# Kernel tuning notes

Hardware: AMD Instinct MI355X
Metric: run time of the kernel (lower is better)

The kernel has to match this reference:

```python
import jax, jax.numpy as jnp
import numpy as np

GROUP_SIZE = 128
NIBBLES = 8  # int4 values packed per int32


def dequantize(qweight, qzeros, scales):
    """Unpack int4 weights/zeros and dequantize: w = (q - z) * scale.

    qweight: [in/8, out] int32, 8 int4 values packed along the IN dim.
    qzeros:  [groups, out/8] int32, 8 int4 zeros packed along the OUT dim.
    scales:  [groups, out] fp16.
    Returns w: [in, out] fp16.
    """
    shifts = (jnp.arange(NIBBLES, dtype=jnp.int32) * 4)
    # unpack weights along input dim -> [in/8, 8, out] -> [in, out]
    q = ((qweight[:, None, :] >> shifts[None, :, None]) & 15)
    q = q.reshape(-1, qweight.shape[1])
    # unpack zeros along output dim -> [groups, out/8, 8] -> [groups, out]
    z = ((qzeros[:, :, None] >> shifts[None, None, :]) & 15)
    z = z.reshape(qzeros.shape[0], -1)
    # broadcast per-group zeros/scales to per-input-row
    z_full = jnp.repeat(z, GROUP_SIZE, axis=0).astype(scales.dtype)   # [in, out]
    s_full = jnp.repeat(scales, GROUP_SIZE, axis=0)                    # [in, out]
    return (q.astype(scales.dtype) - z_full) * s_full


def setup_inputs() -> dict:
    key = jax.random.key(0)
    k1, k2, k3, k4, k5 = jax.random.split(key, 5)
    B, S, IN, OUT, G = 2, 2048, 4096, 11008, 32
    x = jax.random.normal(k1, (B, S, IN), dtype=jnp.float16)
    qweight = jax.random.randint(k2, (IN // 8, OUT), 0, 2147483647, dtype=jnp.int32)
    qzeros = jax.random.randint(k3, (G, OUT // 8), 0, 2147483647, dtype=jnp.int32)
    scales = jax.random.uniform(k4, (G, OUT), dtype=jnp.float16, minval=0.001, maxval=0.02)
    bias = jax.random.normal(k5, (OUT,), dtype=jnp.float16)
    return {"x": x, "qweight": qweight, "qzeros": qzeros, "scales": scales, "bias": bias}


def reference(x, qweight, qzeros, scales, bias):
    w = dequantize(qweight, qzeros, scales)  # [in, out] fp16
    # q4_matmul accumulates in fp32, emits fp16
    out = jnp.einsum('bsi,io->bso', x, w, preferred_element_type=jnp.float32)
    out = out.astype(jnp.float16) + bias
    return out
```

## Files before the change

kernel.cpp:

```cpp
#include <hip/hip_runtime.h>
#include <cstdint>
#include <cstddef>


typedef unsigned short u16;
typedef u16    u16x8  __attribute__((ext_vector_type(8)));
typedef __bf16 bfv8   __attribute__((ext_vector_type(8)));
typedef float  f32x4  __attribute__((ext_vector_type(4)));

#define K_DIM 4096
#define N_DIM 11008
#define GS    128
#define KT    (K_DIM / 64)
#define LSTR  72

__device__ __forceinline__ u16 f2bf(float f) {
  union { float f; uint32_t u; } v;
  v.f = f;
  uint32_t u = v.u + 0x7FFFu + ((v.u >> 16) & 1u);
  return (u16)(u >> 16);
}
__device__ __forceinline__ float f16r(float v) {
  return (float)(_Float16)v;
}
__device__ __forceinline__ void async_load16(const u16* g, u16* l) {
  __builtin_amdgcn_global_load_lds(
      (const __attribute__((address_space(1))) uint32_t*)g,
      (__attribute__((address_space(3))) uint32_t*)l, 16, 0, 0);
}

__global__ __launch_bounds__(256) void convert_x_tiled(
    const float* __restrict__ x, u16* __restrict__ xb) {
  const int kt = blockIdx.x, mt = blockIdx.y;
  const int k0 = kt * 64, m0 = mt * 128;
  u16* dst = xb + ((size_t)(mt * KT + kt)) * 8192;
#pragma unroll
  for (int i = 0; i < 4; ++i) {
    const int g  = i * 256 + threadIdx.x;
    const int nl = g >> 3;
    const int cg = (g & 7) ^ (nl & 7);
    const float* sp = x + (size_t)(m0 + nl) * K_DIM + (k0 + cg * 8);
    const f32x4 p = *(const f32x4*)sp;
    const f32x4 q = *(const f32x4*)(sp + 4);
    u16x8 o;
#pragma unroll
    for (int t = 0; t < 4; ++t) { o[t] = f2bf(p[t]); o[t + 4] = f2bf(q[t]); }
    *(u16x8*)(dst + (size_t)g * 8) = o;
  }
}

__global__ __launch_bounds__(256) void dequant_tiled(
    const uint32_t* __restrict__ qweight, const uint32_t* __restrict__ qzeros,
    const float* __restrict__ scales, u16* __restrict__ wt) {
  const int kt = blockIdx.x, nt = blockIdx.y;
  const int k0 = kt * 64, n0 = nt * 128;
  const int gq = kt >> 1;
  u16* dst = wt + ((size_t)(nt * KT + kt)) * 8192;
#pragma unroll
  for (int i = 0; i < 4; ++i) {
    const int g  = i * 256 + threadIdx.x;
    const int nl = g >> 3;
    const int cg = (g & 7) ^ (nl & 7);
    const int n  = n0 + nl;
    const uint32_t zq = qzeros[(size_t)gq * (N_DIM / 8) + (n >> 3)];
    const int   z   = (int)((zq >> ((n & 7) * 4)) & 15u);
    const float s   = scales[(size_t)gq * N_DIM + n];
    const float nzs = -s * (float)z;
    const uint32_t q = qweight[(size_t)(k0 / 8 + cg) * N_DIM + n];
    u16x8 o;
#pragma unroll
    for (int t = 0; t < 8; ++t) {
      const int qv = (int)((q >> (t * 4)) & 15u);
      o[t] = f2bf(fmaf((float)qv, s, nzs));
    }
    *(u16x8*)(dst + (size_t)g * 8) = o;
  }
}

__global__ __launch_bounds__(256) void gemm_tiled(
    const u16* __restrict__ xb, const u16* __restrict__ wt,
    const float* __restrict__ bias, float* __restrict__ out) {
  __shared__ __align__(16) u16 As[8192];
  __shared__ __align__(16) u16 Bs[8192];

  const int tid  = threadIdx.x;
  const int lane = tid & 63;
  const int wave = tid >> 6;
  const int n0 = blockIdx.x * 128;
  const int m0 = blockIdx.y * 128;

  const int m_off = (wave >> 1) * 64;
  const int n_off = (wave & 1) * 64;
  const int lrow  = lane & 15;
  const int lk    = lane >> 4;
  const int sw    = lrow & 7;

  const u16* abase = xb + (size_t)blockIdx.y * KT * 8192;
  const u16* bbase = wt + (size_t)blockIdx.x * KT * 8192;

  f32x4 acc[4][4];
#pragma unroll
  for (int i = 0; i < 4; ++i)
#pragma unroll
    for (int j = 0; j < 4; ++j) acc[i][j] = f32x4{0.f, 0.f, 0.f, 0.f};

  for (int kt = 0; kt < KT; ++kt) {
    const u16* ag = abase + (size_t)kt * 8192;
    const u16* bg = bbase + (size_t)kt * 8192;
#pragma unroll
    for (int i = 0; i < 4; ++i) {
      async_load16(ag + (size_t)(i * 256 + tid) * 8,
                   As + (size_t)(i * 256 + wave * 64) * 8);
      async_load16(bg + (size_t)(i * 256 + tid) * 8,
                   Bs + (size_t)(i * 256 + wave * 64) * 8);
    }
    __syncthreads();

#pragma unroll
    for (int ks = 0; ks < 2; ++ks) {
      const int kq = ks * 4 + lk;
      const int c = (kq ^ sw) * 8;
      bfv8 a[4], b[4];
#pragma unroll
      for (int i = 0; i < 4; ++i) {
        const int mf = m_off + i * 16 + lrow;
        a[i] = __builtin_bit_cast(bfv8, *(const u16x8*)&As[mf * 64 + c]);
      }
#pragma unroll
      for (int j = 0; j < 4; ++j) {
        const int nf = n_off + j * 16 + lrow;
        b[j] = __builtin_bit_cast(bfv8, *(const u16x8*)&Bs[nf * 64 + c]);
      }
#pragma unroll
      for (int i = 0; i < 4; ++i)
#pragma unroll
        for (int j = 0; j < 4; ++j)
          acc[i][j] = __builtin_amdgcn_mfma_f32_16x16x32_bf16(a[i], b[j],
                                                              acc[i][j], 0, 0, 0);
    }
    __syncthreads();
  }

#pragma unroll
  for (int j = 0; j < 4; ++j) {
    const int n = n0 + n_off + j * 16 + lrow;
    const float bvf = bias[n];
#pragma unroll
    for (int i = 0; i < 4; ++i) {
      const int mrow = m0 + m_off + i * 16 + lk * 4;
#pragma unroll
      for (int r = 0; r < 4; ++r) {
        out[(size_t)(mrow + r) * N_DIM + n] = f16r(f16r(acc[i][j][r]) + bvf);
      }
    }
  }
}

__global__ __launch_bounds__(256) void gemm_fused(
    const float* __restrict__ xf, const uint32_t* __restrict__ qw,
    const uint32_t* __restrict__ qzeros, const float* __restrict__ scales,
    const float* __restrict__ bias, float* __restrict__ out) {
  __shared__ __align__(16) u16 As[128 * LSTR];
  __shared__ __align__(16) u16 Bs[128 * LSTR];

  const int tid  = threadIdx.x;
  const int lane = tid & 63;
  const int wave = tid >> 6;
  const int n0 = blockIdx.x * 128;
  const int m0 = blockIdx.y * 128;
  const int m_off = (wave >> 1) * 64;
  const int n_off = (wave & 1) * 64;
  const int lrow  = lane & 15;
  const int lk    = lane >> 4;
  const int sm = tid >> 3;
  const int sc = tid & 7;

  f32x4 acc[4][4];
#pragma unroll
  for (int i = 0; i < 4; ++i)
#pragma unroll
    for (int j = 0; j < 4; ++j) acc[i][j] = f32x4{0.f, 0.f, 0.f, 0.f};

  const int ncol = n0 + (tid & 127);
  float s_cur = 0.f, nzs_cur = 0.f;

  for (int kt = 0; kt < KT; ++kt) {
    const int k0 = kt * 64;
    u16x8 av[4];
#pragma unroll
    for (int i = 0; i < 4; ++i) {
      const int m = i * 32 + sm;
      const float* sp = xf + (size_t)(m0 + m) * K_DIM + (k0 + sc * 8);
      const f32x4 p = *(const f32x4*)sp;
      const f32x4 q4 = *(const f32x4*)(sp + 4);
#pragma unroll
      for (int t = 0; t < 4; ++t) { av[i][t] = f2bf(p[t]); av[i][t+4] = f2bf(q4[t]); }
    }
    u16x8 bv[4];
    if ((k0 & (GS - 1)) == 0) {
      const int g = k0 >> 7;
      const uint32_t zq = qzeros[(size_t)g * (N_DIM / 8) + (ncol >> 3)];
      const int z = (int)((zq >> ((ncol & 7) * 4)) & 15u);
      s_cur = scales[(size_t)g * N_DIM + ncol];
      nzs_cur = -s_cur * (float)z;
    }
#pragma unroll
    for (int i = 0; i < 4; ++i) {
      const int k8l = (tid >> 7) + i * 2;
      const uint32_t q = qw[(size_t)(k0 / 8 + k8l) * N_DIM + ncol];
#pragma unroll
      for (int t = 0; t < 8; ++t) {
        const int qv = (int)((q >> (t * 4)) & 15u);
        bv[i][t] = f2bf(fmaf((float)qv, s_cur, nzs_cur));
      }
    }
#pragma unroll
    for (int i = 0; i < 4; ++i)
      *(u16x8*)&As[(i * 32 + sm) * LSTR + sc * 8] = av[i];
    {
      const int nl = tid & 127;
#pragma unroll
      for (int i = 0; i < 4; ++i) {
        const int k8l = (tid >> 7) + i * 2;
        *(u16x8*)&Bs[nl * LSTR + k8l * 8] = bv[i];
      }
    }
    __syncthreads();
#pragma unroll
    for (int ks = 0; ks < 2; ++ks) {
      const int c = (ks * 4 + lk) * 8;
      bfv8 a[4], b[4];
#pragma unroll
      for (int i = 0; i < 4; ++i)
        a[i] = __builtin_bit_cast(bfv8,
                 *(const u16x8*)&As[(m_off + i * 16 + lrow) * LSTR + c]);
#pragma unroll
      for (int j = 0; j < 4; ++j)
        b[j] = __builtin_bit_cast(bfv8,
                 *(const u16x8*)&Bs[(n_off + j * 16 + lrow) * LSTR + c]);
#pragma unroll
      for (int i = 0; i < 4; ++i)
#pragma unroll
        for (int j = 0; j < 4; ++j)
          acc[i][j] = __builtin_amdgcn_mfma_f32_16x16x32_bf16(a[i], b[j],
                                                              acc[i][j], 0, 0, 0);
    }
    __syncthreads();
  }
#pragma unroll
  for (int j = 0; j < 4; ++j) {
    const int n = n0 + n_off + j * 16 + lrow;
    const float bvf = bias[n];
#pragma unroll
    for (int i = 0; i < 4; ++i) {
      const int mrow = m0 + m_off + i * 16 + lk * 4;
#pragma unroll
      for (int r = 0; r < 4; ++r)
        out[(size_t)(mrow + r) * N_DIM + n] = f16r(f16r(acc[i][j][r]) + bvf);
    }
  }
}

extern "C" void kernel_launch(void* const* d_in, const int* in_sizes, int n_in,
                              void* d_out, int out_size, void* d_ws, size_t ws_size,
                              hipStream_t stream) {
  const float* x = nullptr;      const uint32_t* qweight = nullptr;
  const uint32_t* qzeros = nullptr;
  const float* scales = nullptr; const float* bias = nullptr;
  int M = 4096;
  for (int i = 0; i < n_in; ++i) {
    const long long s = in_sizes[i];
    if      (s == (long long)(K_DIM / 8) * N_DIM) qweight = (const uint32_t*)d_in[i];
    else if (s == (long long)(K_DIM / GS) * (N_DIM / 8)) qzeros = (const uint32_t*)d_in[i];
    else if (s == (long long)(K_DIM / GS) * N_DIM) scales = (const float*)d_in[i];
    else if (s == (long long)N_DIM) bias = (const float*)d_in[i];
    else { x = (const float*)d_in[i]; M = (int)(s / K_DIM); }
  }
  float* out = (float*)d_out;

  const size_t xb_bytes = (size_t)M * K_DIM * sizeof(u16);
  const size_t wt_bytes = (size_t)N_DIM * K_DIM * sizeof(u16);

  if (ws_size >= xb_bytes + wt_bytes) {
    u16* xbp = (u16*)d_ws;
    u16* wtp = (u16*)((char*)d_ws + xb_bytes);
    convert_x_tiled<<<dim3(KT, M / 128), 256, 0, stream>>>(x, xbp);
    dequant_tiled<<<dim3(KT, N_DIM / 128), 256, 0, stream>>>(
        qweight, qzeros, scales, wtp);
    gemm_tiled<<<dim3(N_DIM / 128, M / 128), 256, 0, stream>>>(
        xbp, wtp, bias, out);
  } else {
    gemm_fused<<<dim3(N_DIM / 128, M / 128), 256, 0, stream>>>(
        x, qweight, qzeros, scales, bias, out);
  }
}
```

Baseline: 741.8 us.

## Use 256x256 GEMM tiles with a four-stage async LDS pipeline

Measured after the change: 620.8 us. 16.3% less time.

```diff
diff --git a/kernel.cpp b/kernel.cpp
--- a/kernel.cpp
+++ b/kernel.cpp
@@ -11,7 +11,7 @@
 #define K_DIM 4096
 #define N_DIM 11008
 #define GS    128
-#define KT    (K_DIM / 64)
+#define KT32  (K_DIM / 32)
 #define LSTR  72
 
 __device__ __forceinline__ u16 f2bf(float f) {
@@ -29,17 +29,17 @@
       (__attribute__((address_space(3))) uint32_t*)l, 16, 0, 0);
 }
 
-__global__ __launch_bounds__(256) void convert_x_tiled(
+__global__ __launch_bounds__(256) void convert_x32(
     const float* __restrict__ x, u16* __restrict__ xb) {
   const int kt = blockIdx.x, mt = blockIdx.y;
-  const int k0 = kt * 64, m0 = mt * 128;
-  u16* dst = xb + ((size_t)(mt * KT + kt)) * 8192;
-#pragma unroll
-  for (int i = 0; i < 4; ++i) {
-    const int g  = i * 256 + threadIdx.x;
-    const int nl = g >> 3;
-    const int cg = (g & 7) ^ (nl & 7);
-    const float* sp = x + (size_t)(m0 + nl) * K_DIM + (k0 + cg * 8);
+  const int m0 = mt * 128, k0 = kt * 32;
+  u16* dst = xb + ((size_t)mt * KT32 + kt) * 4096;
+#pragma unroll
+  for (int i = 0; i < 2; ++i) {
+    const int g = i * 256 + threadIdx.x;
+    const int r = g >> 2, s = g & 3;
+    const int kq = s ^ ((r >> 1) & 3);
+    const float* sp = x + (size_t)(m0 + r) * K_DIM + (k0 + kq * 8);
     const f32x4 p = *(const f32x4*)sp;
     const f32x4 q = *(const f32x4*)(sp + 4);
     u16x8 o;
@@ -49,105 +49,132 @@
   }
 }
 
-__global__ __launch_bounds__(256) void dequant_tiled(
+__global__ __launch_bounds__(256) void dequant32(
     const uint32_t* __restrict__ qweight, const uint32_t* __restrict__ qzeros,
     const float* __restrict__ scales, u16* __restrict__ wt) {
   const int kt = blockIdx.x, nt = blockIdx.y;
-  const int k0 = kt * 64, n0 = nt * 128;
-  const int gq = kt >> 1;
-  u16* dst = wt + ((size_t)(nt * KT + kt)) * 8192;
-#pragma unroll
-  for (int i = 0; i < 4; ++i) {
-    const int g  = i * 256 + threadIdx.x;
-    const int nl = g >> 3;
-    const int cg = (g & 7) ^ (nl & 7);
-    const int n  = n0 + nl;
+  const int n0 = nt * 128;
+  const int gq = kt >> 2;
+  u16* dst = wt + ((size_t)nt * KT32 + kt) * 4096;
+#pragma unroll
+  for (int i = 0; i < 2; ++i) {
+    const int g = i * 256 + threadIdx.x;
+    const int r = g >> 2, s = g & 3;
+    const int kq = s ^ ((r >> 1) & 3);
+    const int n = n0 + r;
     const uint32_t zq = qzeros[(size_t)gq * (N_DIM / 8) + (n >> 3)];
     const int   z   = (int)((zq >> ((n & 7) * 4)) & 15u);
-    const float s   = scales[(size_t)gq * N_DIM + n];
-    const float nzs = -s * (float)z;
-    const uint32_t q = qweight[(size_t)(k0 / 8 + cg) * N_DIM + n];
+    const float sc  = scales[(size_t)gq * N_DIM + n];
+    const float nzs = -sc * (float)z;
+    const uint32_t q = qweight[(size_t)(kt * 4 + kq) * N_DIM + n];
     u16x8 o;
 #pragma unroll
     for (int t = 0; t < 8; ++t) {
       const int qv = (int)((q >> (t * 4)) & 15u);
-      o[t] = f2bf(fmaf((float)qv, s, nzs));
+      o[t] = f2bf(fmaf((float)qv, sc, nzs));
     }
     *(u16x8*)(dst + (size_t)g * 8) = o;
   }
 }
 
-__global__ __launch_bounds__(256) void gemm_tiled(
+#define STAGE_A(t) do {                                                      \
+    const int sb_ = (t) & 3;                                                 \
+    async_load16(atile + ((size_t)0 * KT32 + (t)) * 4096 + tid * 8,          \
+                 As + sb_ * 8192 + 0 * 4096 + wave * 512);                   \
+    async_load16(atile + ((size_t)1 * KT32 + (t)) * 4096 + tid * 8,          \
+                 As + sb_ * 8192 + 1 * 4096 + wave * 512);                   \
+  } while (0)
+#define STAGE_B(t) do {                                                      \
+    const int sb_ = (t) & 3;                                                 \
+    async_load16(btile + ((size_t)0 * KT32 + (t)) * 4096 + tid * 8,          \
+                 Bs + sb_ * 8192 + 0 * 4096 + wave * 512);                   \
+    async_load16(btile + ((size_t)1 * KT32 + (t)) * 4096 + tid * 8,          \
+                 Bs + sb_ * 8192 + 1 * 4096 + wave * 512);                   \
+  } while (0)
+#define LDF(base, off) __builtin_bit_cast(bfv8, *(const u16x8*)((base) + (off)))
+#define MF(i, j, av, bv)                                                     \
+  acc[i][j] = __builtin_amdgcn_mfma_f32_16x16x32_bf16((av), (bv), acc[i][j], 0, 0, 0)
+
+__global__ __launch_bounds__(512, 2) void gemm_256(
     const u16* __restrict__ xb, const u16* __restrict__ wt,
     const float* __restrict__ bias, float* __restrict__ out) {
-  __shared__ __align__(16) u16 As[8192];
-  __shared__ __align__(16) u16 Bs[8192];
+  __shared__ __align__(16) u16 As[4 * 8192];
+  __shared__ __align__(16) u16 Bs[4 * 8192];
 
   const int tid  = threadIdx.x;
   const int lane = tid & 63;
   const int wave = tid >> 6;
-  const int n0 = blockIdx.x * 128;
-  const int m0 = blockIdx.y * 128;
-
-  const int m_off = (wave >> 1) * 64;
-  const int n_off = (wave & 1) * 64;
-  const int lrow  = lane & 15;
-  const int lk    = lane >> 4;
-  const int sw    = lrow & 7;
-
-  const u16* abase = xb + (size_t)blockIdx.y * KT * 8192;
-  const u16* bbase = wt + (size_t)blockIdx.x * KT * 8192;
-
-  f32x4 acc[4][4];
-#pragma unroll
-  for (int i = 0; i < 4; ++i)
+  const int wm   = wave >> 2;
+  const int wn   = wave & 3;
+  const int lrow = lane & 15;
+  const int lk   = lane >> 4;
+  const int swz  = (lrow >> 1) & 3;
+
+  const int n0 = blockIdx.x * 256;
+  const int m0 = blockIdx.y * 256;
+
+  const u16* atile = xb + (size_t)(2 * blockIdx.y) * KT32 * 4096;
+  const u16* btile = wt + (size_t)(2 * blockIdx.x) * KT32 * 4096;
+
+  const int aoff = wm * 4096 + (lrow * 4 + (lk ^ swz)) * 8;
+  const int boff = (wn >> 1) * 4096 + (((wn & 1) * 64 + lrow) * 4 + (lk ^ swz)) * 8;
+
+  f32x4 acc[8][4];
+#pragma unroll
+  for (int i = 0; i < 8; ++i)
 #pragma unroll
     for (int j = 0; j < 4; ++j) acc[i][j] = f32x4{0.f, 0.f, 0.f, 0.f};
 
-  for (int kt = 0; kt < KT; ++kt) {
-    const u16* ag = abase + (size_t)kt * 8192;
-    const u16* bg = bbase + (size_t)kt * 8192;
-#pragma unroll
-    for (int i = 0; i < 4; ++i) {
-      async_load16(ag + (size_t)(i * 256 + tid) * 8,
-                   As + (size_t)(i * 256 + wave * 64) * 8);
-      async_load16(bg + (size_t)(i * 256 + tid) * 8,
-                   Bs + (size_t)(i * 256 + wave * 64) * 8);
-    }
-    __syncthreads();
-
-#pragma unroll
-    for (int ks = 0; ks < 2; ++ks) {
-      const int kq = ks * 4 + lk;
-      const int c = (kq ^ sw) * 8;
-      bfv8 a[4], b[4];
-#pragma unroll
-      for (int i = 0; i < 4; ++i) {
-        const int mf = m_off + i * 16 + lrow;
-        a[i] = __builtin_bit_cast(bfv8, *(const u16x8*)&As[mf * 64 + c]);
-      }
-#pragma unroll
-      for (int j = 0; j < 4; ++j) {
-        const int nf = n_off + j * 16 + lrow;
-        b[j] = __builtin_bit_cast(bfv8, *(const u16x8*)&Bs[nf * 64 + c]);
-      }
-#pragma unroll
-      for (int i = 0; i < 4; ++i)
-#pragma unroll
-        for (int j = 0; j < 4; ++j)
-          acc[i][j] = __builtin_amdgcn_mfma_f32_16x16x32_bf16(a[i], b[j],
-                                                              acc[i][j], 0, 0, 0);
-    }
-    __syncthreads();
+  STAGE_A(0); STAGE_B(0); STAGE_A(1); STAGE_B(1); STAGE_A(2); STAGE_B(2);
+  asm volatile("s_waitcnt vmcnt(8)" ::: "memory");
+  asm volatile("s_barrier" ::: "memory");
+
+#pragma unroll 4
+  for (int t = 0; t < KT32; ++t) {
+    const u16* A = As + (t & 3) * 8192;
+    const u16* B = Bs + (t & 3) * 8192;
+    bfv8 a[4], b[4];
+#pragma unroll
+    for (int j = 0; j < 4; ++j) b[j] = LDF(B, boff + j * 512);
+#pragma unroll
+    for (int i = 0; i < 4; ++i) a[i] = LDF(A, aoff + i * 512);
+    if (t + 3 < KT32) STAGE_A(t + 3);
+    asm volatile("s_barrier" ::: "memory");
+    __builtin_amdgcn_s_setprio(1);
+#pragma unroll
+    for (int i = 0; i < 4; ++i)
+#pragma unroll
+      for (int j = 0; j < 4; ++j) MF(i, j, a[i], b[j]);
+    __builtin_amdgcn_s_setprio(0);
+    asm volatile("s_barrier" ::: "memory");
+#pragma unroll
+    for (int i = 0; i < 4; ++i) a[i] = LDF(A, aoff + (4 + i) * 512);
+    if (t + 3 < KT32) STAGE_B(t + 3);
+    asm volatile("s_barrier" ::: "memory");
+    __builtin_amdgcn_s_setprio(1);
+#pragma unroll
+    for (int i = 0; i < 4; ++i)
+#pragma unroll
+      for (int j = 0; j < 4; ++j) MF(4 + i, j, a[i], b[j]);
+    __builtin_amdgcn_s_setprio(0);
+    if (t == KT32 - 1) break;
+    if (t < KT32 - 3) {
+      asm volatile("s_waitcnt vmcnt(8)" ::: "memory");
+    } else if (t == KT32 - 3) {
+      asm volatile("s_waitcnt vmcnt(4)" ::: "memory");
+    } else {
+      asm volatile("s_waitcnt vmcnt(0)" ::: "memory");
+    }
+    asm volatile("s_barrier" ::: "memory");
   }
 
 #pragma unroll
   for (int j = 0; j < 4; ++j) {
-    const int n = n0 + n_off + j * 16 + lrow;
+    const int n = n0 + wn * 64 + j * 16 + lrow;
     const float bvf = bias[n];
 #pragma unroll
-    for (int i = 0; i < 4; ++i) {
-      const int mrow = m0 + m_off + i * 16 + lk * 4;
+    for (int i = 0; i < 8; ++i) {
+      const int mrow = m0 + wm * 128 + i * 16 + lk * 4;
 #pragma unroll
       for (int r = 0; r < 4; ++r) {
         out[(size_t)(mrow + r) * N_DIM + n] = f16r(f16r(acc[i][j][r]) + bvf);
@@ -184,7 +211,7 @@
   const int ncol = n0 + (tid & 127);
   float s_cur = 0.f, nzs_cur = 0.f;
 
-  for (int kt = 0; kt < KT; ++kt) {
+  for (int kt = 0; kt < K_DIM / 64; ++kt) {
     const int k0 = kt * 64;
     u16x8 av[4];
 #pragma unroll
@@ -281,16 +308,16 @@
   const size_t xb_bytes = (size_t)M * K_DIM * sizeof(u16);
   const size_t wt_bytes = (size_t)N_DIM * K_DIM * sizeof(u16);
 
-  if (ws_size >= xb_bytes + wt_bytes) {
+  if (ws_size >= xb_bytes + wt_bytes && (M % 256) == 0) {
     u16* xbp = (u16*)d_ws;
     u16* wtp = (u16*)((char*)d_ws + xb_bytes);
-    convert_x_tiled<<<dim3(KT, M / 128), 256, 0, stream>>>(x, xbp);
-    dequant_tiled<<<dim3(KT, N_DIM / 128), 256, 0, stream>>>(
+    convert_x32<<<dim3(KT32, M / 128), 256, 0, stream>>>(x, xbp);
+    dequant32<<<dim3(KT32, N_DIM / 128), 256, 0, stream>>>(
         qweight, qzeros, scales, wtp);
-    gemm_tiled<<<dim3(N_DIM / 128, M / 128), 256, 0, stream>>>(
+    gemm_256<<<dim3(N_DIM / 256, M / 256), 512, 0, stream>>>(
         xbp, wtp, bias, out);
   } else {
-    gemm_fused<<<dim3(N_DIM / 128, M / 128), 256, 0, stream>>>(
+    gemm_fused<<<dim3(N_DIM / 128, (M + 127) / 128), 256, 0, stream>>>(
         x, qweight, qzeros, scales, bias, out);
   }
 }
```

## Replace 128x128 GEMM with double-buffered 256x256 pipelined MFMA kernel

Applied to the files above, without the earlier changes.

Measured after the change: 614.3 us. 1.21x faster.

```diff
diff --git a/kernel.cpp b/kernel.cpp
--- a/kernel.cpp
+++ b/kernel.cpp
@@ -11,7 +11,7 @@
 #define K_DIM 4096
 #define N_DIM 11008
 #define GS    128
-#define KT    (K_DIM / 64)
+#define KT64  (K_DIM / 64)
 #define LSTR  72
 
 __device__ __forceinline__ u16 f2bf(float f) {
@@ -33,7 +33,7 @@
     const float* __restrict__ x, u16* __restrict__ xb) {
   const int kt = blockIdx.x, mt = blockIdx.y;
   const int k0 = kt * 64, m0 = mt * 128;
-  u16* dst = xb + ((size_t)(mt * KT + kt)) * 8192;
+  u16* dst = xb + ((size_t)(mt * KT64 + kt)) * 8192;
 #pragma unroll
   for (int i = 0; i < 4; ++i) {
     const int g  = i * 256 + threadIdx.x;
@@ -53,9 +53,9 @@
     const uint32_t* __restrict__ qweight, const uint32_t* __restrict__ qzeros,
     const float* __restrict__ scales, u16* __restrict__ wt) {
   const int kt = blockIdx.x, nt = blockIdx.y;
-  const int k0 = kt * 64, n0 = nt * 128;
+  const int n0 = nt * 128;
   const int gq = kt >> 1;
-  u16* dst = wt + ((size_t)(nt * KT + kt)) * 8192;
+  u16* dst = wt + ((size_t)(nt * KT64 + kt)) * 8192;
 #pragma unroll
   for (int i = 0; i < 4; ++i) {
     const int g  = i * 256 + threadIdx.x;
@@ -66,7 +66,7 @@
     const int   z   = (int)((zq >> ((n & 7) * 4)) & 15u);
     const float s   = scales[(size_t)gq * N_DIM + n];
     const float nzs = -s * (float)z;
-    const uint32_t q = qweight[(size_t)(k0 / 8 + cg) * N_DIM + n];
+    const uint32_t q = qweight[(size_t)(kt * 8 + cg) * N_DIM + n];
     u16x8 o;
 #pragma unroll
     for (int t = 0; t < 8; ++t) {
@@ -77,77 +77,125 @@
   }
 }
 
-__global__ __launch_bounds__(256) void gemm_tiled(
+#define LDF(p) __builtin_bit_cast(bfv8, *(const u16x8*)(p))
+#define BAR()  asm volatile("s_barrier" ::: "memory")
+#define VMW(n) asm volatile("s_waitcnt vmcnt(" #n ")" ::: "memory")
+
+#define STAGE_AH(ktt, h) do {                                                 \
+    const u16* s_ = at0 + ((size_t)(h) * KT64 + (ktt)) * 8192;                \
+    u16* d_ = &As[(((ktt) & 1) * 16384) + (h) * 8192 + wave * 512];           \
+    async_load16(s_ + (size_t)tid * 8, d_);                                   \
+    async_load16(s_ + (size_t)(512 + tid) * 8, d_ + 4096);                    \
+  } while (0)
+#define STAGE_BH(ktt, h) do {                                                 \
+    const u16* s_ = bt0 + ((size_t)(h) * KT64 + (ktt)) * 8192;                \
+    u16* d_ = &Bs[(((ktt) & 1) * 16384) + (h) * 8192 + wave * 512];           \
+    async_load16(s_ + (size_t)tid * 8, d_);                                   \
+    async_load16(s_ + (size_t)(512 + tid) * 8, d_ + 4096);                    \
+  } while (0)
+
+#define RD_AP(v, ib, sbx) do {                                                \
+    v[0] = LDF(&As[(sbx) * 16384 + aoff + (ib) * 1024 + kq0]);                \
+    v[1] = LDF(&As[(sbx) * 16384 + aoff + (ib) * 1024 + kq1]);                \
+    v[2] = LDF(&As[(sbx) * 16384 + aoff + ((ib) + 1) * 1024 + kq0]);          \
+    v[3] = LDF(&As[(sbx) * 16384 + aoff + ((ib) + 1) * 1024 + kq1]);          \
+  } while (0)
+#define RD_B8(v, sbx) do {                                                    \
+    _Pragma("unroll")                                                         \
+    for (int j_ = 0; j_ < 4; ++j_) {                                          \
+      v[2 * j_]     = LDF(&Bs[(sbx) * 16384 + boff + j_ * 1024 + kq0]);       \
+      v[2 * j_ + 1] = LDF(&Bs[(sbx) * 16384 + boff + j_ * 1024 + kq1]);       \
+    }                                                                         \
+  } while (0)
+
+#define MM(ib, av, bv) do {                                                   \
+    __builtin_amdgcn_s_setprio(1);                                            \
+    _Pragma("unroll")                                                         \
+    for (int ks_ = 0; ks_ < 2; ++ks_)                                         \
+      _Pragma("unroll")                                                       \
+      for (int ii_ = 0; ii_ < 2; ++ii_)                                       \
+        _Pragma("unroll")                                                     \
+        for (int j_ = 0; j_ < 4; ++j_)                                        \
+          acc[(ib) + ii_][j_] = __builtin_amdgcn_mfma_f32_16x16x32_bf16(      \
+              av[2 * ii_ + ks_], bv[2 * j_ + ks_], acc[(ib) + ii_][j_],       \
+              0, 0, 0);                                                       \
+    __builtin_amdgcn_s_setprio(0);                                            \
+  } while (0)
+
+#define KTILE_BODY(kt, sb, bcur, bnxt) do {                                   \
+    RD_AP(a23, 2, sb);  STAGE_AH((kt) + 1, 0);  MM(0, a01, bcur);  BAR();     \
+    RD_AP(a45, 4, sb);  STAGE_AH((kt) + 1, 1);  MM(2, a23, bcur);  BAR();     \
+    RD_AP(a67, 6, sb);  STAGE_BH((kt) + 2, 0);  MM(4, a45, bcur);             \
+    VMW(2);  BAR();                                                           \
+    RD_B8(bnxt, (sb) ^ 1);  RD_AP(a01, 0, (sb) ^ 1);  STAGE_BH((kt) + 2, 1);  \
+    MM(6, a67, bcur);  BAR();                                                 \
+  } while (0)
+
+__global__ __launch_bounds__(512, 2) void gemm_256(
     const u16* __restrict__ xb, const u16* __restrict__ wt,
     const float* __restrict__ bias, float* __restrict__ out) {
-  __shared__ __align__(16) u16 As[8192];
-  __shared__ __align__(16) u16 Bs[8192];
+  __shared__ __align__(16) u16 As[2 * 16384];
+  __shared__ __align__(16) u16 Bs[2 * 16384];
 
   const int tid  = threadIdx.x;
   const int lane = tid & 63;
   const int wave = tid >> 6;
-  const int n0 = blockIdx.x * 128;
-  const int m0 = blockIdx.y * 128;
-
-  const int m_off = (wave >> 1) * 64;
-  const int n_off = (wave & 1) * 64;
-  const int lrow  = lane & 15;
-  const int lk    = lane >> 4;
-  const int sw    = lrow & 7;
-
-  const u16* abase = xb + (size_t)blockIdx.y * KT * 8192;
-  const u16* bbase = wt + (size_t)blockIdx.x * KT * 8192;
-
-  f32x4 acc[4][4];
-#pragma unroll
-  for (int i = 0; i < 4; ++i)
+  const int wm   = wave >> 2;
+  const int wn   = wave & 3;
+  const int lrow = lane & 15;
+  const int lk   = lane >> 4;
+  const int swz  = lrow & 7;
+
+  const int nwg = gridDim.x * gridDim.y;
+  int wg = blockIdx.y * gridDim.x + blockIdx.x;
+  if ((nwg & 7) == 0) wg = (wg & 7) * (nwg >> 3) + (wg >> 3);
+  const int bx = wg % gridDim.x;
+  const int by = wg / gridDim.x;
+  const int n0 = bx * 256;
+  const int m0 = by * 256;
+
+  const u16* at0 = xb + (size_t)(2 * by) * KT64 * 8192;
+  const u16* bt0 = wt + (size_t)(2 * bx) * KT64 * 8192;
+
+  const int aoff = wm * 8192 + lrow * 64;
+  const int boff = (wn >> 1) * 8192 + ((wn & 1) * 64 + lrow) * 64;
+  const int kq0  = (lk ^ swz) * 8;
+  const int kq1  = ((4 + lk) ^ swz) * 8;
+
+  bfv8 a01[4], a23[4], a45[4], a67[4], bA[8], bB[8];
+  f32x4 acc[8][4];
+#pragma unroll
+  for (int i = 0; i < 8; ++i)
 #pragma unroll
     for (int j = 0; j < 4; ++j) acc[i][j] = f32x4{0.f, 0.f, 0.f, 0.f};
 
-  for (int kt = 0; kt < KT; ++kt) {
-    const u16* ag = abase + (size_t)kt * 8192;
-    const u16* bg = bbase + (size_t)kt * 8192;
-#pragma unroll
-    for (int i = 0; i < 4; ++i) {
-      async_load16(ag + (size_t)(i * 256 + tid) * 8,
-                   As + (size_t)(i * 256 + wave * 64) * 8);
-      async_load16(bg + (size_t)(i * 256 + tid) * 8,
-                   Bs + (size_t)(i * 256 + wave * 64) * 8);
-    }
-    __syncthreads();
-
-#pragma unroll
-    for (int ks = 0; ks < 2; ++ks) {
-      const int kq = ks * 4 + lk;
-      const int c = (kq ^ sw) * 8;
-      bfv8 a[4], b[4];
-#pragma unroll
-      for (int i = 0; i < 4; ++i) {
-        const int mf = m_off + i * 16 + lrow;
-        a[i] = __builtin_bit_cast(bfv8, *(const u16x8*)&As[mf * 64 + c]);
-      }
-#pragma unroll
-      for (int j = 0; j < 4; ++j) {
-        const int nf = n_off + j * 16 + lrow;
-        b[j] = __builtin_bit_cast(bfv8, *(const u16x8*)&Bs[nf * 64 + c]);
-      }
-#pragma unroll
-      for (int i = 0; i < 4; ++i)
-#pragma unroll
-        for (int j = 0; j < 4; ++j)
-          acc[i][j] = __builtin_amdgcn_mfma_f32_16x16x32_bf16(a[i], b[j],
-                                                              acc[i][j], 0, 0, 0);
-    }
-    __syncthreads();
-  }
+  STAGE_AH(0, 0); STAGE_AH(0, 1); STAGE_BH(0, 0); STAGE_BH(0, 1);
+  STAGE_BH(1, 0); STAGE_BH(1, 1);
+  VMW(4); BAR();
+  RD_B8(bA, 0); RD_AP(a01, 0, 0);
+
+#pragma unroll 1
+  for (int kt2 = 0; kt2 < 31; ++kt2) {
+    const int kt = 2 * kt2;
+    KTILE_BODY(kt,     0, bA, bB);
+    KTILE_BODY(kt + 1, 1, bB, bA);
+  }
+  RD_AP(a23, 2, 0);  STAGE_AH(63, 0);  MM(0, a01, bA);  BAR();
+  RD_AP(a45, 4, 0);  STAGE_AH(63, 1);  MM(2, a23, bA);  BAR();
+  RD_AP(a67, 6, 0);                    MM(4, a45, bA);  VMW(0); BAR();
+  RD_B8(bB, 1); RD_AP(a01, 0, 1);      MM(6, a67, bA);  BAR();
+  RD_AP(a23, 2, 1);  MM(0, a01, bB);  BAR();
+  RD_AP(a45, 4, 1);  MM(2, a23, bB);  BAR();
+  RD_AP(a67, 6, 1);  MM(4, a45, bB);  BAR();
+                     MM(6, a67, bB);
 
 #pragma unroll
   for (int j = 0; j < 4; ++j) {
-    const int n = n0 + n_off + j * 16 + lrow;
+    const int n = n0 + wn * 64 + j * 16 + lrow;
     const float bvf = bias[n];
 #pragma unroll
-    for (int i = 0; i < 4; ++i) {
-      const int mrow = m0 + m_off + i * 16 + lk * 4;
+    for (int i = 0; i < 8; ++i) {
+      const int mrow = m0 + wm * 128 + i * 16 + lk * 4;
 #pragma unroll
       for (int r = 0; r < 4; ++r) {
         out[(size_t)(mrow + r) * N_DIM + n] = f16r(f16r(acc[i][j][r]) + bvf);
@@ -184,7 +232,7 @@
   const int ncol = n0 + (tid & 127);
   float s_cur = 0.f, nzs_cur = 0.f;
 
-  for (int kt = 0; kt < KT; ++kt) {
+  for (int kt = 0; kt < K_DIM / 64; ++kt) {
     const int k0 = kt * 64;
     u16x8 av[4];
 #pragma unroll
@@ -281,16 +329,16 @@
   const size_t xb_bytes = (size_t)M * K_DIM * sizeof(u16);
   const size_t wt_bytes = (size_t)N_DIM * K_DIM * sizeof(u16);
 
-  if (ws_size >= xb_bytes + wt_bytes) {
+  if (ws_size >= xb_bytes + wt_bytes && (M % 256) == 0) {
     u16* xbp = (u16*)d_ws;
     u16* wtp = (u16*)((char*)d_ws + xb_bytes);
-    convert_x_tiled<<<dim3(KT, M / 128), 256, 0, stream>>>(x, xbp);
-    dequant_tiled<<<dim3(KT, N_DIM / 128), 256, 0, stream>>>(
+    convert_x_tiled<<<dim3(KT64, M / 128), 256, 0, stream>>>(x, xbp);
+    dequant_tiled<<<dim3(KT64, N_DIM / 128), 256, 0, stream>>>(
         qweight, qzeros, scales, wtp);
-    gemm_tiled<<<dim3(N_DIM / 128, M / 128), 256, 0, stream>>>(
+    gemm_256<<<dim3(N_DIM / 256, M / 256), 512, 0, stream>>>(
         xbp, wtp, bias, out);
   } else {
-    gemm_fused<<<dim3(N_DIM / 128, M / 128), 256, 0, stream>>>(
+    gemm_fused<<<dim3(N_DIM / 128, (M + 127) / 128), 256, 0, stream>>>(
         x, qweight, qzeros, scales, bias, out);
   }
 }
```
